# Performance work log

Measured on AMD Instinct MI355X. Metric: run time of the kernel, lower is better.

Reference implementation:

```python
import jax, jax.numpy as jnp
import numpy as np
from jax import lax

DN = ('NCHW', 'OIHW', 'NCHW')

def dsconv(x, dw_w, dw_b, pw_w, pw_b, dilation):
    # depthwise 3x3 (groups = C), padding = dilation, then pointwise 1x1
    C = x.shape[1]
    y = lax.conv_general_dilated(
        x, dw_w, window_strides=(1, 1),
        padding=[(dilation, dilation), (dilation, dilation)],
        rhs_dilation=(dilation, dilation),
        dimension_numbers=DN, feature_group_count=C)
    y = y + dw_b[None, :, None, None]
    y = lax.conv_general_dilated(y, pw_w, window_strides=(1, 1), padding='VALID',
                                 dimension_numbers=DN)
    return y + pw_b[None, :, None, None]


def setup_inputs() -> dict:
    key = jax.random.key(0)
    ks = jax.random.split(key, 16)
    B, C, H, W = 4, 256, 64, 64
    R = C // 8  # reduced_channels = 32
    s = 0.05
    inp = {
        'x': jax.random.normal(ks[0], (B, C, H, W), dtype=jnp.float32),
        # conv1 (dilation 1)
        'c1_dw_w': jax.random.normal(ks[1], (C, 1, 3, 3), dtype=jnp.float32) * s,
        'c1_dw_b': jax.random.normal(ks[2], (C,), dtype=jnp.float32) * s,
        'c1_pw_w': jax.random.normal(ks[3], (R, C, 1, 1), dtype=jnp.float32) * s,
        'c1_pw_b': jax.random.normal(ks[4], (R,), dtype=jnp.float32) * s,
        # conv2 (dilation 3)
        'c2_dw_w': jax.random.normal(ks[5], (C, 1, 3, 3), dtype=jnp.float32) * s,
        'c2_dw_b': jax.random.normal(ks[6], (C,), dtype=jnp.float32) * s,
        'c2_pw_w': jax.random.normal(ks[7], (R, C, 1, 1), dtype=jnp.float32) * s,
        'c2_pw_b': jax.random.normal(ks[8], (R,), dtype=jnp.float32) * s,
        # conv3 (dilation 5)
        'c3_dw_w': jax.random.normal(ks[9], (C, 1, 3, 3), dtype=jnp.float32) * s,
        'c3_dw_b': jax.random.normal(ks[10], (C,), dtype=jnp.float32) * s,
        'c3_pw_w': jax.random.normal(ks[11], (R, C, 1, 1), dtype=jnp.float32) * s,
        'c3_pw_b': jax.random.normal(ks[12], (R,), dtype=jnp.float32) * s,
        # conv_out 1x1: R -> C
        'co_w': jax.random.normal(ks[13], (C, R, 1, 1), dtype=jnp.float32) * s,
        'co_b': jax.random.normal(ks[14], (C,), dtype=jnp.float32) * s,
    }
    return inp


def reference(x, c1_dw_w, c1_dw_b, c1_pw_w, c1_pw_b,
              c2_dw_w, c2_dw_b, c2_pw_w, c2_pw_b,
              c3_dw_w, c3_dw_b, c3_pw_w, c3_pw_b,
              co_w, co_b):
    B, C, H, W = x.shape
    R = C // 8
    N = H * W
    Fp1 = dsconv(x, c1_dw_w, c1_dw_b, c1_pw_w, c1_pw_b, 1).reshape(B, R, N)
    Fp2 = dsconv(x, c2_dw_w, c2_dw_b, c2_pw_w, c2_pw_b, 3).reshape(B, R, N)
    Fp3 = dsconv(x, c3_dw_w, c3_dw_b, c3_pw_w, c3_pw_b, 5).reshape(B, R, N)
    # Mpam[b,i,j] = sum_c Fp2[b,c,i] * Fp3[b,c,j]; softmax over j
    Mpam = jax.nn.softmax(jnp.einsum('bci,bcj->bij', Fp2, Fp3), axis=-1)
    # Fpmap[b,c,i] = sum_j Fp1[b,c,j] * Mpam[i,j]  (matmul with Mpam^T)
    Fpmap = jnp.einsum('bcj,bij->bci', Fp1, Mpam).reshape(B, R, H, W)
    Fpmap = lax.conv_general_dilated(Fpmap, co_w, (1, 1), 'VALID',
                                     dimension_numbers=DN) + co_b[None, :, None, None]
    return x + Fpmap
```

## Files before the change

### kernel.cpp

```cpp
#include <hip/hip_runtime.h>
#include <stdint.h>

#define BB 4
#define CC 256
#define NN 4096
#define RR 32
#define NCHUNK 8
#define JSTEPS (NN / NCHUNK / 32)
#define CSIZE  (NN / NCHUNK)

typedef __attribute__((ext_vector_type(8)))  short  short8;
typedef __attribute__((ext_vector_type(4)))  short  short4v;
typedef __attribute__((ext_vector_type(16))) float  floatx16;

static __device__ __forceinline__ unsigned short f2bf(float f) {
    union { float f; unsigned int u; } v; v.f = f;
    unsigned int u = v.u;
    u += 0x7fffu + ((u >> 16) & 1u);
    return (unsigned short)(u >> 16);
}

static __device__ __forceinline__ float bf2f(unsigned short u) {
    union { unsigned int u; float f; } v; v.u = ((unsigned int)u) << 16;
    return v.f;
}

static __device__ __forceinline__ float exp2_fast(float x) {
#if __has_builtin(__builtin_amdgcn_exp2f)
    return __builtin_amdgcn_exp2f(x);
#else
    return exp2f(x);
#endif
}

__global__ __launch_bounds__(256, 4) void k_dw(
    const float* __restrict__ x,
    const float* __restrict__ w1, const float* __restrict__ b1,
    const float* __restrict__ w2, const float* __restrict__ b2,
    const float* __restrict__ w3, const float* __restrict__ b3,
    unsigned short* __restrict__ Dq)
{
    int t = threadIdx.x, lane = t & 63, wv = t >> 6;
    int c = blockIdx.x, b = blockIdx.y;
    int hb = wv * 16;
    const float* xc = x + ((size_t)(b * CC + c)) * NN;
    float row[26];
    #pragma unroll
    for (int k = 0; k < 26; k++) {
        int rr = hb - 5 + k;
        int rc = rr < 0 ? 0 : (rr > 63 ? 63 : rr);
        float v = xc[rc * 64 + lane];
        row[k] = (rr >= 0 && rr <= 63) ? v : 0.f;
    }
    const float* DWW[3] = {w1, w2, w3};
    const float* DWB[3] = {b1, b2, b3};
    #pragma unroll
    for (int p = 0; p < 3; p++) {
        const int d = (p == 0) ? 1 : (p == 1 ? 3 : 5);
        float wt[9];
        #pragma unroll
        for (int q = 0; q < 9; q++) wt[q] = DWW[p][c * 9 + q];
        float bias = DWB[p][c];
        bool okl = lane >= d, okr = lane < 64 - d;
        int lml = okl ? lane - d : 0;
        int lpr = okr ? lane + d : 63;
        float sm[26], sp[26];
        #pragma unroll
        for (int k = 5 - d; k <= 20 + d; k++) {
            float a = __shfl(row[k], lml, 64); sm[k] = okl ? a : 0.f;
            float q2 = __shfl(row[k], lpr, 64); sp[k] = okr ? q2 : 0.f;
        }
        unsigned short* Dp = Dq + (((size_t)p * BB + b) * CC + c) * NN;
        #pragma unroll
        for (int hl = 0; hl < 16; hl++) {
            int k0 = hl + 5 - d, k1 = hl + 5, k2 = hl + 5 + d;
            float o = bias
                + wt[0] * sm[k0] + wt[1] * row[k0] + wt[2] * sp[k0]
                + wt[3] * sm[k1] + wt[4] * row[k1] + wt[5] * sp[k1]
                + wt[6] * sm[k2] + wt[7] * row[k2] + wt[8] * sp[k2];
            Dp[(hb + hl) * 64 + lane] = f2bf(o);
        }
    }
}

__global__ __launch_bounds__(256, 4) void k_pw(
    const unsigned short* __restrict__ Dq,
    const float* __restrict__ p1, const float* __restrict__ pb1,
    const float* __restrict__ p2, const float* __restrict__ pb2,
    const float* __restrict__ p3, const float* __restrict__ pb3,
    unsigned short* __restrict__ V, unsigned short* __restrict__ Qt,
    unsigned short* __restrict__ Kt)
{
    __shared__ unsigned short PW[32 * 264];
    __shared__ unsigned short Lt[4][32][40];
    int t = threadIdx.x, lane = t & 63, l31 = lane & 31, h = lane >> 5, wv = t >> 6;
    int ntile = blockIdx.x, p = blockIdx.y, b = blockIdx.z;
    const float* pw  = (p == 0) ? p1  : (p == 1 ? p2  : p3);
    const float* pwb = (p == 0) ? pb1 : (p == 1 ? pb2 : pb3);

    {
        int r = t >> 3, cb0 = (t & 7) * 32;
        const float4* src = (const float4*)(pw + r * CC + cb0);
        #pragma unroll
        for (int g = 0; g < 8; g++) {
            float4 f = src[g];
            short4v s4;
            s4[0] = (short)f2bf(f.x); s4[1] = (short)f2bf(f.y);
            s4[2] = (short)f2bf(f.z); s4[3] = (short)f2bf(f.w);
            *(short4v*)&PW[r * 264 + cb0 + g * 4] = s4;
        }
    }
    __syncthreads();

    int n = ntile * 128 + wv * 32 + l31;
    const unsigned short* Dn = Dq + (((size_t)p * BB + b) * CC + 8 * h) * NN + n;
    floatx16 acc = {};
    #pragma unroll 4
    for (int kt = 0; kt < 16; kt++) {
        short8 af = *(const short8*)&PW[l31 * 264 + kt * 16 + 8 * h];
        short8 bf;
        #pragma unroll
        for (int j = 0; j < 8; j++) bf[j] = (short)Dn[(size_t)(kt * 16 + j) * NN];
        acc = __builtin_amdgcn_mfma_f32_32x32x16_bf16(af, bf, acc, 0, 0, 0);
    }

    if (p == 0) {
        #pragma unroll
        for (int rr = 0; rr < 16; rr++) {
            int r = (rr & 3) + 8 * (rr >> 2) + 4 * h;
            V[((size_t)(b * RR + r)) * NN + n] = f2bf(acc[rr] + pwb[r]);
        }
    } else {
        const float sc = (p == 1) ? 1.4426950408889634f : 1.f;
        unsigned short* outp = (p == 1) ? Qt : Kt;
        #pragma unroll
        for (int rr = 0; rr < 16; rr++) {
            int r = (rr & 3) + 8 * (rr >> 2) + 4 * h;
            Lt[wv][l31][r] = f2bf((acc[rr] + pwb[r]) * sc);
        }
        __threadfence_block();
        unsigned short* orow = outp + ((size_t)b * NN + n) * RR + h * 16;
        short8 lo = *(const short8*)&Lt[wv][l31][h * 16];
        *(short8*)orow = lo;
        short8 hi = *(const short8*)&Lt[wv][l31][h * 16 + 8];
        *(short8*)(orow + 8) = hi;
    }
}

__global__ __launch_bounds__(256, 4) void k_attn(
    const unsigned short* __restrict__ Qt, const unsigned short* __restrict__ Kt,
    const unsigned short* __restrict__ V, float* __restrict__ OP, float* __restrict__ LP)
{
    __shared__ unsigned short Vt[32][36];
    int t = threadIdx.x;
    int wave = t >> 6, lane = t & 63, l31 = lane & 31, h = lane >> 5;
    int itile = blockIdx.x * 4 + wave;
    int chunk = blockIdx.y;
    int b = blockIdx.z;
    int i = itile * 32 + l31;

    const short8* qrow = (const short8*)(Qt + ((size_t)b * NN + i) * RR);
    short8 q1 = qrow[h], q2 = qrow[2 + h];

    const unsigned short* Kb = Kt + (size_t)b * NN * RR;
    const unsigned short* Vb = V + (size_t)b * RR * NN;

    int sr = t >> 3, sc = t & 7;
    const unsigned short* vsrc = Vb + (size_t)sr * NN + chunk * CSIZE + sc * 4;

    floatx16 acc = {};
    float lacc = 0.f;

    short4v vreg = *(const short4v*)vsrc;
    const short8* krow0 = (const short8*)(Kb + (size_t)(chunk * CSIZE + l31) * RR);
    short8 ka1 = krow0[h], ka2 = krow0[2 + h];

    for (int js = 0; js < JSTEPS; js++) {
        __syncthreads();
        *(short4v*)(&Vt[sr][sc * 4]) = vreg;
        int jn = (js + 1 < JSTEPS) ? js + 1 : js;
        vreg = *(const short4v*)(vsrc + jn * 32);
        __syncthreads();

        floatx16 st = {};
        st = __builtin_amdgcn_mfma_f32_32x32x16_bf16(ka1, q1, st, 0, 0, 0);
        st = __builtin_amdgcn_mfma_f32_32x32x16_bf16(ka2, q2, st, 0, 0, 0);
        const short8* krow = (const short8*)(Kb + (size_t)(chunk * CSIZE + jn * 32 + l31) * RR);
        ka1 = krow[h]; ka2 = krow[2 + h];

        float p[16];
        #pragma unroll
        for (int r = 0; r < 16; r++) { p[r] = exp2_fast(st[r]); lacc += p[r]; }
        short8 pa1, pa2;
        #pragma unroll
        for (int r = 0; r < 8; r++) {
            pa1[r] = (short)f2bf(p[r]);
            pa2[r] = (short)f2bf(p[r + 8]);
        }
        const unsigned short* vrow = &Vt[l31][0];
        short4v v0 = *(const short4v*)(vrow + 4 * h);
        short4v v1 = *(const short4v*)(vrow + 8 + 4 * h);
        short4v v2 = *(const short4v*)(vrow + 16 + 4 * h);
        short4v v3 = *(const short4v*)(vrow + 24 + 4 * h);
        short8 vb1, vb2;
        #pragma unroll
        for (int q = 0; q < 4; q++) {
            vb1[q] = v0[q]; vb1[q + 4] = v1[q];
            vb2[q] = v2[q]; vb2[q + 4] = v3[q];
        }
        acc = __builtin_amdgcn_mfma_f32_32x32x16_bf16(pa1, vb1, acc, 0, 0, 0);
        acc = __builtin_amdgcn_mfma_f32_32x32x16_bf16(pa2, vb2, acc, 0, 0, 0);
    }
    size_t slot = ((size_t)(b * 128 + itile) * NCHUNK + chunk) * 64 + lane;
    float* op = OP + slot * 16;
    #pragma unroll
    for (int r = 0; r < 16; r++) op[r] = acc[r];
    LP[slot] = lacc;
}

__global__ void k_merge(const float* __restrict__ OP, const float* __restrict__ LP,
                        unsigned short* __restrict__ FMt) {
    int itile = blockIdx.x, b = blockIdx.y;
    int lane = threadIdx.x, l31 = lane & 31, h = lane >> 5;
    __shared__ float linv[32];
    size_t base = (size_t)(b * 128 + itile) * NCHUNK;
    float ls = 0.f;
    #pragma unroll
    for (int ch = 0; ch < NCHUNK; ch++) ls += LP[(base + ch) * 64 + lane];
    ls += __shfl_xor(ls, 32, 64);
    if (lane < 32) linv[lane] = 1.f / ls;
    __syncthreads();
    float o[16];
    #pragma unroll
    for (int r = 0; r < 16; r++) o[r] = 0.f;
    for (int ch = 0; ch < NCHUNK; ch++) {
        const float* op = OP + ((base + ch) * 64 + lane) * 16;
        #pragma unroll
        for (int r = 0; r < 16; r++) o[r] += op[r];
    }
    int ibase = itile * 32;
    #pragma unroll
    for (int r = 0; r < 16; r++) {
        int il = (r & 3) + 8 * (r >> 2) + 4 * h;
        FMt[((size_t)b * NN + (ibase + il)) * RR + l31] = f2bf(o[r] * linv[il]);
    }
}

__global__ __launch_bounds__(256, 4) void k_convout(
    const float* __restrict__ x, const unsigned short* __restrict__ FMt,
    const float* __restrict__ cw, const float* __restrict__ cb,
    float* __restrict__ out)
{
    int t = threadIdx.x, lane = t & 63, l31 = lane & 31, h = lane >> 5, wv = t >> 6;
    int ng = blockIdx.x, ct = blockIdx.y, b = blockIdx.z;
    int n0 = ng * 128 + wv * 32;
    int co0 = ct * 32;
    const float* cwp = cw + (size_t)(co0 + l31) * RR + 8 * h;
    short8 a1, a2;
    #pragma unroll
    for (int j = 0; j < 8; j++) {
        a1[j] = (short)f2bf(cwp[j]);
        a2[j] = (short)f2bf(cwp[16 + j]);
    }
    const unsigned short* fp = FMt + ((size_t)b * NN + n0 + l31) * RR + 8 * h;
    short8 b1 = *(const short8*)fp;
    short8 b2 = *(const short8*)(fp + 16);
    floatx16 acc = {};
    acc = __builtin_amdgcn_mfma_f32_32x32x16_bf16(a1, b1, acc, 0, 0, 0);
    acc = __builtin_amdgcn_mfma_f32_32x32x16_bf16(a2, b2, acc, 0, 0, 0);
    #pragma unroll
    for (int rr = 0; rr < 16; rr++) {
        int co = co0 + (rr & 3) + 8 * (rr >> 2) + 4 * h;
        size_t o = ((size_t)(b * CC + co)) * NN + n0 + l31;
        out[o] = x[o] + acc[rr] + cb[co];
    }
}

extern "C" void kernel_launch(void* const* d_in, const int* in_sizes, int n_in,
                              void* d_out, int out_size, void* d_ws, size_t ws_size,
                              hipStream_t stream) {
    const float* x = (const float*)d_in[0];
    char* ws = (char*)d_ws;
    unsigned short* Dq = (unsigned short*)(ws);
    float*          OP = (float*)(ws);
    unsigned short* Qt = (unsigned short*)(ws + 25165824);
    unsigned short* Kt = (unsigned short*)(ws + 26214400);
    unsigned short* V  = (unsigned short*)(ws + 27262976);
    float*          LP = (float*)(ws + 28311552);
    unsigned short* FMt= (unsigned short*)(ws + 29360128);

    hipLaunchKernelGGL(k_dw, dim3(CC, BB), dim3(256), 0, stream, x,
                       (const float*)d_in[1], (const float*)d_in[2],
                       (const float*)d_in[5], (const float*)d_in[6],
                       (const float*)d_in[9], (const float*)d_in[10], Dq);
    hipLaunchKernelGGL(k_pw, dim3(32, 3, BB), dim3(256), 0, stream, Dq,
                       (const float*)d_in[3], (const float*)d_in[4],
                       (const float*)d_in[7], (const float*)d_in[8],
                       (const float*)d_in[11], (const float*)d_in[12],
                       V, Qt, Kt);
    hipLaunchKernelGGL(k_attn, dim3(32, NCHUNK, BB), dim3(256), 0, stream, Qt, Kt, V, OP, LP);
    hipLaunchKernelGGL(k_merge, dim3(128, BB), dim3(64), 0, stream, OP, LP, FMt);
    hipLaunchKernelGGL(k_convout, dim3(32, 8, BB), dim3(256), 0, stream,
                       x, FMt, (const float*)d_in[13], (const float*)d_in[14], (float*)d_out);
}
```

Measured before the change: 144.8 us.

## Fuse merge with output conv, double-buffer V tile, use packed bf16 conversion

Merges the chunk-reduction kernel and the 1x1 output conv into one kernel, so the normalized attention output stays in shared memory instead of making a bf16 round trip through global memory, and one launch is removed. The attention kernel now double-buffers the V tile in shared memory, cutting two barriers per step to one. Software bf16 rounding is replaced by the packed hardware conversion builtin where the compiler provides it. The fused kernel re-converts the conv weights per block and has only 512 blocks, and the builtin's rounding may differ slightly from the software routine.

```diff
diff --git a/kernel.cpp b/kernel.cpp
--- a/kernel.cpp
+++ b/kernel.cpp
@@ -13,16 +13,38 @@
 typedef __attribute__((ext_vector_type(4)))  short  short4v;
 typedef __attribute__((ext_vector_type(16))) float  floatx16;
 
-static __device__ __forceinline__ unsigned short f2bf(float f) {
+#if defined(__has_builtin)
+#if __has_builtin(__builtin_amdgcn_cvt_pk_bf16_f32)
+#define HAVE_PK_BF16 1
+#endif
+#endif
+
+#ifdef HAVE_PK_BF16
+typedef __attribute__((ext_vector_type(2))) __bf16 bf16x2;
+#endif
+
+static __device__ __forceinline__ unsigned short f2bf_sw(float f) {
     union { float f; unsigned int u; } v; v.f = f;
     unsigned int u = v.u;
     u += 0x7fffu + ((u >> 16) & 1u);
     return (unsigned short)(u >> 16);
 }
 
-static __device__ __forceinline__ float bf2f(unsigned short u) {
-    union { unsigned int u; float f; } v; v.u = ((unsigned int)u) << 16;
-    return v.f;
+static __device__ __forceinline__ unsigned int pk_bf16(float a, float b) {
+#ifdef HAVE_PK_BF16
+    bf16x2 r = __builtin_amdgcn_cvt_pk_bf16_f32(a, b);
+    unsigned int u; __builtin_memcpy(&u, &r, 4); return u;
+#else
+    return (unsigned int)f2bf_sw(a) | ((unsigned int)f2bf_sw(b) << 16);
+#endif
+}
+
+static __device__ __forceinline__ unsigned short f2bf(float f) {
+#ifdef HAVE_PK_BF16
+    return (unsigned short)(pk_bf16(f, 0.f) & 0xffffu);
+#else
+    return f2bf_sw(f);
+#endif
 }
 
 static __device__ __forceinline__ float exp2_fast(float x) {
@@ -104,10 +126,10 @@
         #pragma unroll
         for (int g = 0; g < 8; g++) {
             float4 f = src[g];
-            short4v s4;
-            s4[0] = (short)f2bf(f.x); s4[1] = (short)f2bf(f.y);
-            s4[2] = (short)f2bf(f.z); s4[3] = (short)f2bf(f.w);
-            *(short4v*)&PW[r * 264 + cb0 + g * 4] = s4;
+            union { short4v s; unsigned int u[2]; } s4;
+            s4.u[0] = pk_bf16(f.x, f.y);
+            s4.u[1] = pk_bf16(f.z, f.w);
+            *(short4v*)&PW[r * 264 + cb0 + g * 4] = s4.s;
         }
     }
     __syncthreads();
@@ -151,7 +173,7 @@
     const unsigned short* __restrict__ Qt, const unsigned short* __restrict__ Kt,
     const unsigned short* __restrict__ V, float* __restrict__ OP, float* __restrict__ LP)
 {
-    __shared__ unsigned short Vt[32][36];
+    __shared__ unsigned short Vt[2][32][36];
     int t = threadIdx.x;
     int wave = t >> 6, lane = t & 63, l31 = lane & 31, h = lane >> 5;
     int itile = blockIdx.x * 4 + wave;
@@ -171,33 +193,34 @@
     floatx16 acc = {};
     float lacc = 0.f;
 
-    short4v vreg = *(const short4v*)vsrc;
+    *(short4v*)(&Vt[0][sr][sc * 4]) = *(const short4v*)vsrc;
+    short4v vnext = *(const short4v*)(vsrc + 32);
     const short8* krow0 = (const short8*)(Kb + (size_t)(chunk * CSIZE + l31) * RR);
     short8 ka1 = krow0[h], ka2 = krow0[2 + h];
+    __syncthreads();
 
     for (int js = 0; js < JSTEPS; js++) {
-        __syncthreads();
-        *(short4v*)(&Vt[sr][sc * 4]) = vreg;
-        int jn = (js + 1 < JSTEPS) ? js + 1 : js;
-        vreg = *(const short4v*)(vsrc + jn * 32);
-        __syncthreads();
+        int cur = js & 1;
+        if (js + 1 < JSTEPS) *(short4v*)(&Vt[1 - cur][sr][sc * 4]) = vnext;
+        if (js + 2 < JSTEPS) vnext = *(const short4v*)(vsrc + (js + 2) * 32);
 
         floatx16 st = {};
         st = __builtin_amdgcn_mfma_f32_32x32x16_bf16(ka1, q1, st, 0, 0, 0);
         st = __builtin_amdgcn_mfma_f32_32x32x16_bf16(ka2, q2, st, 0, 0, 0);
+        int jn = (js + 1 < JSTEPS) ? js + 1 : js;
         const short8* krow = (const short8*)(Kb + (size_t)(chunk * CSIZE + jn * 32 + l31) * RR);
         ka1 = krow[h]; ka2 = krow[2 + h];
 
         float p[16];
         #pragma unroll
         for (int r = 0; r < 16; r++) { p[r] = exp2_fast(st[r]); lacc += p[r]; }
-        short8 pa1, pa2;
-        #pragma unroll
-        for (int r = 0; r < 8; r++) {
-            pa1[r] = (short)f2bf(p[r]);
-            pa2[r] = (short)f2bf(p[r + 8]);
-        }
-        const unsigned short* vrow = &Vt[l31][0];
+        union { short8 s; unsigned int u[4]; } pa1, pa2;
+        #pragma unroll
+        for (int r = 0; r < 8; r += 2) {
+            pa1.u[r >> 1] = pk_bf16(p[r], p[r + 1]);
+            pa2.u[r >> 1] = pk_bf16(p[r + 8], p[r + 9]);
+        }
+        const unsigned short* vrow = &Vt[cur][l31][0];
         short4v v0 = *(const short4v*)(vrow + 4 * h);
         short4v v1 = *(const short4v*)(vrow + 8 + 4 * h);
         short4v v2 = *(const short4v*)(vrow + 16 + 4 * h);
@@ -208,8 +231,9 @@
             vb1[q] = v0[q]; vb1[q + 4] = v1[q];
             vb2[q] = v2[q]; vb2[q + 4] = v3[q];
         }
-        acc = __builtin_amdgcn_mfma_f32_32x32x16_bf16(pa1, vb1, acc, 0, 0, 0);
-        acc = __builtin_amdgcn_mfma_f32_32x32x16_bf16(pa2, vb2, acc, 0, 0, 0);
+        acc = __builtin_amdgcn_mfma_f32_32x32x16_bf16(pa1.s, vb1, acc, 0, 0, 0);
+        acc = __builtin_amdgcn_mfma_f32_32x32x16_bf16(pa2.s, vb2, acc, 0, 0, 0);
+        __syncthreads();
     }
     size_t slot = ((size_t)(b * 128 + itile) * NCHUNK + chunk) * 64 + lane;
     float* op = OP + slot * 16;
@@ -218,61 +242,78 @@
     LP[slot] = lacc;
 }
 
-__global__ void k_merge(const float* __restrict__ OP, const float* __restrict__ LP,
-                        unsigned short* __restrict__ FMt) {
+__global__ __launch_bounds__(256, 4) void k_out(
+    const float* __restrict__ x, const float* __restrict__ OP,
+    const float* __restrict__ LP, const float* __restrict__ cw,
+    const float* __restrict__ cb, float* __restrict__ out)
+{
+    __shared__ float linv[32];
+    __shared__ unsigned short Ft[32][36];
+    __shared__ unsigned short CW[256 * 36];
+    int t = threadIdx.x, lane = t & 63, l31 = lane & 31, h = lane >> 5, wv = t >> 6;
     int itile = blockIdx.x, b = blockIdx.y;
-    int lane = threadIdx.x, l31 = lane & 31, h = lane >> 5;
-    __shared__ float linv[32];
     size_t base = (size_t)(b * 128 + itile) * NCHUNK;
-    float ls = 0.f;
-    #pragma unroll
-    for (int ch = 0; ch < NCHUNK; ch++) ls += LP[(base + ch) * 64 + lane];
-    ls += __shfl_xor(ls, 32, 64);
-    if (lane < 32) linv[lane] = 1.f / ls;
+
+    {
+        const float4* src = (const float4*)(cw + (size_t)t * RR);
+        #pragma unroll
+        for (int g = 0; g < 8; g++) {
+            float4 f = src[g];
+            union { short4v s; unsigned int u[2]; } s4;
+            s4.u[0] = pk_bf16(f.x, f.y);
+            s4.u[1] = pk_bf16(f.z, f.w);
+            *(short4v*)&CW[t * 36 + g * 4] = s4.s;
+        }
+    }
+    int g = wv;
+    float s0 = 0.f, s1 = 0.f, s2 = 0.f, s3 = 0.f;
+    #pragma unroll
+    for (int ch = 0; ch < NCHUNK; ch++) {
+        const float4 v = *(const float4*)(OP + ((base + ch) * 64 + lane) * 16 + 4 * g);
+        s0 += v.x; s1 += v.y; s2 += v.z; s3 += v.w;
+    }
+    if (t < 32) {
+        float sl = 0.f;
+        #pragma unroll
+        for (int ch = 0; ch < NCHUNK; ch++) {
+            sl += LP[(base + ch) * 64 + t] + LP[(base + ch) * 64 + t + 32];
+        }
+        linv[t] = 1.f / sl;
+    }
     __syncthreads();
-    float o[16];
-    #pragma unroll
-    for (int r = 0; r < 16; r++) o[r] = 0.f;
-    for (int ch = 0; ch < NCHUNK; ch++) {
-        const float* op = OP + ((base + ch) * 64 + lane) * 16;
-        #pragma unroll
-        for (int r = 0; r < 16; r++) o[r] += op[r];
-    }
-    int ibase = itile * 32;
-    #pragma unroll
-    for (int r = 0; r < 16; r++) {
-        int il = (r & 3) + 8 * (r >> 2) + 4 * h;
-        FMt[((size_t)b * NN + (ibase + il)) * RR + l31] = f2bf(o[r] * linv[il]);
-    }
-}
-
-__global__ __launch_bounds__(256, 4) void k_convout(
-    const float* __restrict__ x, const unsigned short* __restrict__ FMt,
-    const float* __restrict__ cw, const float* __restrict__ cb,
-    float* __restrict__ out)
-{
-    int t = threadIdx.x, lane = t & 63, l31 = lane & 31, h = lane >> 5, wv = t >> 6;
-    int ng = blockIdx.x, ct = blockIdx.y, b = blockIdx.z;
-    int n0 = ng * 128 + wv * 32;
-    int co0 = ct * 32;
-    const float* cwp = cw + (size_t)(co0 + l31) * RR + 8 * h;
-    short8 a1, a2;
-    #pragma unroll
-    for (int j = 0; j < 8; j++) {
-        a1[j] = (short)f2bf(cwp[j]);
-        a2[j] = (short)f2bf(cwp[16 + j]);
-    }
-    const unsigned short* fp = FMt + ((size_t)b * NN + n0 + l31) * RR + 8 * h;
-    short8 b1 = *(const short8*)fp;
-    short8 b2 = *(const short8*)(fp + 16);
-    floatx16 acc = {};
-    acc = __builtin_amdgcn_mfma_f32_32x32x16_bf16(a1, b1, acc, 0, 0, 0);
-    acc = __builtin_amdgcn_mfma_f32_32x32x16_bf16(a2, b2, acc, 0, 0, 0);
-    #pragma unroll
-    for (int rr = 0; rr < 16; rr++) {
-        int co = co0 + (rr & 3) + 8 * (rr >> 2) + 4 * h;
-        size_t o = ((size_t)(b * CC + co)) * NN + n0 + l31;
-        out[o] = x[o] + acc[rr] + cb[co];
+    {
+        float sv[4] = {s0, s1, s2, s3};
+        #pragma unroll
+        for (int j = 0; j < 4; j++) {
+            int reg = 4 * g + j;
+            int il = (reg & 3) + 8 * (reg >> 2) + 4 * h;
+            Ft[il][l31] = f2bf(sv[j] * linv[il]);
+        }
+    }
+    __syncthreads();
+    #pragma unroll
+    for (int cti = 0; cti < 2; cti++) {
+        int co0 = (wv * 2 + cti) * 32;
+        const unsigned short* arow = &CW[(co0 + l31) * 36 + 8 * h];
+        union { short8 s; short4v hh[2]; } a1, a2, b1, b2;
+        a1.hh[0] = *(const short4v*)arow;
+        a1.hh[1] = *(const short4v*)(arow + 4);
+        a2.hh[0] = *(const short4v*)(arow + 16);
+        a2.hh[1] = *(const short4v*)(arow + 20);
+        const unsigned short* brow = &Ft[l31][8 * h];
+        b1.hh[0] = *(const short4v*)brow;
+        b1.hh[1] = *(const short4v*)(brow + 4);
+        b2.hh[0] = *(const short4v*)(brow + 16);
+        b2.hh[1] = *(const short4v*)(brow + 20);
+        floatx16 acc = {};
+        acc = __builtin_amdgcn_mfma_f32_32x32x16_bf16(a1.s, b1.s, acc, 0, 0, 0);
+        acc = __builtin_amdgcn_mfma_f32_32x32x16_bf16(a2.s, b2.s, acc, 0, 0, 0);
+        #pragma unroll
+        for (int rr = 0; rr < 16; rr++) {
+            int co = co0 + (rr & 3) + 8 * (rr >> 2) + 4 * h;
+            size_t o = ((size_t)(b * CC + co)) * NN + itile * 32 + l31;
+            out[o] = x[o] + acc[rr] + cb[co];
+        }
     }
 }
 
@@ -287,7 +328,6 @@
     unsigned short* Kt = (unsigned short*)(ws + 26214400);
     unsigned short* V  = (unsigned short*)(ws + 27262976);
     float*          LP = (float*)(ws + 28311552);
-    unsigned short* FMt= (unsigned short*)(ws + 29360128);
 
     hipLaunchKernelGGL(k_dw, dim3(CC, BB), dim3(256), 0, stream, x,
                        (const float*)d_in[1], (const float*)d_in[2],
@@ -299,7 +339,7 @@
                        (const float*)d_in[11], (const float*)d_in[12],
                        V, Qt, Kt);
     hipLaunchKernelGGL(k_attn, dim3(32, NCHUNK, BB), dim3(256), 0, stream, Qt, Kt, V, OP, LP);
-    hipLaunchKernelGGL(k_merge, dim3(128, BB), dim3(64), 0, stream, OP, LP, FMt);
-    hipLaunchKernelGGL(k_convout, dim3(32, 8, BB), dim3(256), 0, stream,
-                       x, FMt, (const float*)d_in[13], (const float*)d_in[14], (float*)d_out);
-}
+    hipLaunchKernelGGL(k_out, dim3(128, BB), dim3(256), 0, stream,
+                       x, OP, LP, (const float*)d_in[13], (const float*)d_in[14],
+                       (float*)d_out);
+}
```

New measurement: 143.3 us. Within noise of the previous version (-1.0%).
